# Optimization experiments

Hardware: AMD Instinct MI355X
Metric: run time of the kernel (lower is better)

Reference implementation:

```python
import jax, jax.numpy as jnp
import numpy as np
import math

B, N, M = 4, 512, 64
F, Q, H, R = 256, 16, 8, 32
D = F // H
ETA = 4.0
EPS = 1e-5
FFN_H = 512

def layer_norm(x, g, b):
    mu = jnp.mean(x, axis=-1, keepdims=True)
    var = jnp.mean((x - mu) ** 2, axis=-1, keepdims=True)
    return (x - mu) * jax.lax.rsqrt(var + EPS) * g + b

def setup_inputs() -> dict:
    key = jax.random.key(0)
    ks = jax.random.split(key, 24)
    def xav(k, shape):
        fan_in, fan_out = shape[1], shape[0]
        std = math.sqrt(2.0 / (fan_in + fan_out))
        return jax.random.normal(k, shape, dtype=jnp.float32) * std
    inp = {
        'a': jax.random.normal(ks[0], (B, N, F), dtype=jnp.float32),
        'charges': jax.random.normal(ks[1], (B, N, Q), dtype=jnp.float32),
        'idx_j': jax.random.randint(ks[2], (B, N, M), 0, N),
        'd_ij': jax.random.uniform(ks[3], (B, N, M), dtype=jnp.float32) * 5.0,
        'mask_ij': jax.random.bernoulli(ks[4], 0.3, (B, N, M)),
        'radial_shifts': jnp.linspace(0.5, 5.0, R, dtype=jnp.float32),
        'Wq': xav(ks[5], (F, F + Q)), 'bq': jnp.zeros((F,), jnp.float32),
        'Wk': xav(ks[6], (F, F + Q)), 'bk': jnp.zeros((F,), jnp.float32),
        'Wv': xav(ks[7], (F, F + Q)), 'bv': jnp.zeros((F,), jnp.float32),
        'Wrb': xav(ks[8], (H, R)), 'brb': jnp.zeros((H,), jnp.float32),
        'Wout': xav(ks[9], (F, 2 * F + R)), 'bout': jnp.zeros((F,), jnp.float32),
        'g1': jnp.ones((F,), jnp.float32), 'b1': jnp.zeros((F,), jnp.float32),
        'g2': jnp.ones((F,), jnp.float32), 'b2': jnp.zeros((F,), jnp.float32),
        'Wf1': xav(ks[10], (FFN_H, F)), 'bf1': jnp.zeros((FFN_H,), jnp.float32),
        'Wf2': xav(ks[11], (F, FFN_H)), 'bf2': jnp.zeros((F,), jnp.float32),
    }
    return inp

def reference(a, charges, idx_j, d_ij, mask_ij, radial_shifts,
              Wq, bq, Wk, bk, Wv, bv, Wrb, brb, Wout, bout,
              g1, b1, g2, b2, Wf1, bf1, Wf2, bf2):
    bidx = jnp.arange(B)[:, None, None]
    a_j = a[bidx, idx_j]          # [B,N,M,F]
    q_j = charges[bidx, idx_j]    # [B,N,M,Q]
    center = jnp.concatenate([a, charges], axis=-1)       # [B,N,F+Q]
    neigh = jnp.concatenate([a_j, q_j], axis=-1)          # [B,N,M,F+Q]
    q = (center @ Wq.T + bq).reshape(B, N, H, D)
    k = (neigh @ Wk.T + bk).reshape(B, N, M, H, D)
    v = (neigh @ Wv.T + bv).reshape(B, N, M, H, D)
    # radial basis: exp(-eta*(d - shift)^2)  -> [B,N,M,R]
    radial = jnp.exp(-ETA * (d_ij[..., None] - radial_shifts) ** 2)
    scores = jnp.einsum('bnhd,bnmhd->bnmh', q, k) / math.sqrt(D)
    scores = scores + radial @ Wrb.T + brb                # [B,N,M,H]
    scores = jnp.swapaxes(scores, -1, -2)                 # [B,N,H,M]
    scores = jnp.where(mask_ij[:, :, None, :], -jnp.inf, scores)
    attn = jax.nn.softmax(scores, axis=-1)
    attn = jnp.nan_to_num(attn, nan=0.0, posinf=0.0, neginf=0.0)
    context = jnp.einsum('bnhm,bnmhd->bnhd', attn, v).reshape(B, N, F)
    radial_context = jnp.einsum('bnhm,bnmg->bnhg', attn, radial).mean(axis=-2)  # [B,N,R]
    update = jnp.concatenate([a, context, radial_context], axis=-1) @ Wout.T + bout
    x = layer_norm(a + update, g1, b1)
    ff = jax.nn.gelu(x @ Wf1.T + bf1, approximate=False) @ Wf2.T + bf2
    return layer_norm(x + ff, g2, b2)
```

## Files before the change

kernel.cpp:

```cpp
#include <hip/hip_runtime.h>
#include <hip/hip_bf16.h>
#include <math.h>

#define Bb 4
#define Nn 512
#define Mm 64
#define Ff 256
#define Qq 16
#define Hh 8
#define Rr 32
#define FFNH 512
#define ROWS (Bb*Nn)
#define KIN (Ff+Qq)
#define KINP 288
#define KOUT (2*Ff+Rr)

typedef short short8 __attribute__((ext_vector_type(8)));
typedef unsigned short ushort8 __attribute__((ext_vector_type(8)));
typedef float f32x4 __attribute__((ext_vector_type(4)));

__device__ inline unsigned short f2b(float f) {
    union { float f; unsigned u; } c; c.f = f;
    unsigned r = c.u + 0x7fffu + ((c.u >> 16) & 1u);
    return (unsigned short)(r >> 16);
}
__device__ inline float b2f(unsigned short u) {
    union { unsigned u; float f; } c; c.u = ((unsigned)u) << 16;
    return c.f;
}

#define OFF_CENTER 0
#define OFF_WQKV   (OFF_CENTER + ROWS*KINP)
#define OFF_WOUT   (OFF_WQKV + 768*KINP)
#define OFF_WF1    (OFF_WOUT + Ff*KOUT)
#define OFF_WF2    (OFF_WF1 + FFNH*Ff)
#define OFF_U      (OFF_WF2 + Ff*FFNH)
#define OFF_XB     (OFF_U + ROWS*KOUT)
#define OFF_FFH    (OFF_XB + ROWS*Ff)
#define OFF_QKVB   (OFF_FFH + ROWS*FFNH)
#define CONV_TOTAL OFF_U
#define CONV_BLK4  (CONV_TOTAL/1024)
#define A2U_BLK4   (ROWS*Ff/1024)
#define MSK_BLK16  (Bb*Nn*Mm/(256*16))

__global__ __launch_bounds__(256) void prep(const float* __restrict__ a,
                                            const float* __restrict__ ch,
                                            const float* __restrict__ Wq,
                                            const float* __restrict__ Wk,
                                            const float* __restrict__ Wv,
                                            const float* __restrict__ Wout,
                                            const float* __restrict__ Wf1,
                                            const float* __restrict__ Wf2,
                                            const unsigned char* __restrict__ mask,
                                            int* __restrict__ flag,
                                            unsigned short* __restrict__ arena) {
    int bid = blockIdx.x, tid = threadIdx.x;
    if (bid < CONV_BLK4) {
        int i = (bid * 256 + tid) * 4;
        float4 v4 = {0.f, 0.f, 0.f, 0.f};
        if (i < OFF_WQKV) {
            int row = i / KINP, c = i - row * KINP;
            if (c < Ff)       v4 = *reinterpret_cast<const float4*>(a  + (size_t)row * Ff + c);
            else if (c < KIN) v4 = *reinterpret_cast<const float4*>(ch + (size_t)row * Qq + (c - Ff));
        } else if (i < OFF_WOUT) {
            int j = i - OFF_WQKV;
            int n = j / KINP, c = j - n * KINP;
            const float* W = n < 256 ? Wq : (n < 512 ? Wk : Wv);
            int nr = n & 255;
            if (c < KIN) v4 = *reinterpret_cast<const float4*>(W + (size_t)nr * KIN + c);
        } else if (i < OFF_WF1) {
            v4 = *reinterpret_cast<const float4*>(Wout + (i - OFF_WOUT));
        } else if (i < OFF_WF2) {
            v4 = *reinterpret_cast<const float4*>(Wf1 + (i - OFF_WF1));
        } else {
            v4 = *reinterpret_cast<const float4*>(Wf2 + (i - OFF_WF2));
        }
        ushort4 u;
        u.x = f2b(v4.x); u.y = f2b(v4.y); u.z = f2b(v4.z); u.w = f2b(v4.w);
        *reinterpret_cast<ushort4*>(arena + i) = u;
    } else if (bid < CONV_BLK4 + A2U_BLK4) {
        int j = ((bid - CONV_BLK4) * 256 + tid) * 4;
        int row = j >> 8, col = j & 255;
        float4 v4 = *reinterpret_cast<const float4*>(a + j);
        ushort4 u;
        u.x = f2b(v4.x); u.y = f2b(v4.y); u.z = f2b(v4.z); u.w = f2b(v4.w);
        *reinterpret_cast<ushort4*>(arena + OFF_U + (size_t)row * KOUT + col) = u;
    } else {
        int i = ((bid - CONV_BLK4 - A2U_BLK4) * 256 + tid) * 4;
        const uint4 v = reinterpret_cast<const uint4*>(mask)[i >> 2];
        unsigned m = (v.x | v.y | v.z | v.w) & 0xFFFFFF00u;
        if (m) *flag = 1;
    }
}

template<int KT, int SPLIT, int MODE>
__global__ __launch_bounds__(256) void gemm_mfma(const unsigned short* __restrict__ Ab, int lda,
                                                 const unsigned short* __restrict__ Wb, int ldw,
                                                 const float* __restrict__ b0,
                                                 const float* __restrict__ b1,
                                                 const float* __restrict__ b2,
                                                 float* __restrict__ C,
                                                 unsigned short* __restrict__ Cb,
                                                 int ldc, size_t pstride) {
    __shared__ unsigned short As[2][64][32];
    __shared__ unsigned short Bs[2][64][32];
    int tid = threadIdx.x;
    int colbase = blockIdx.x * 64;
    int rowbase = blockIdx.y * 64;
    constexpr int TPER = (KT + SPLIT - 1) / SPLIT;
    int t0 = blockIdx.z * TPER;
    int NL = KT - t0; if (NL > TPER) NL = TPER;

    int sr = tid >> 2, sl = tid & 3;
    const unsigned short* Ap = Ab + (size_t)(rowbase + sr) * lda + sl * 8;
    const unsigned short* Wp = Wb + (size_t)(colbase + sr) * ldw + sl * 8;
    int ssw = (sl ^ (sr & 3)) * 8;

    int wave = tid >> 6, lane = tid & 63;
    int wr = (wave >> 1) * 32, wc = (wave & 1) * 32;
    int lrow = lane & 15;
    int kslot = lane >> 4;
    int sp = (kslot ^ (lane & 3)) * 8;

    uint4 av, wv;
    auto prefetch = [&](int t) {
        av = *reinterpret_cast<const uint4*>(Ap + (size_t)t * 32);
        wv = *reinterpret_cast<const uint4*>(Wp + (size_t)t * 32);
    };
    auto writeLDS = [&](int buf) {
        *reinterpret_cast<uint4*>(&As[buf][sr][ssw]) = av;
        *reinterpret_cast<uint4*>(&Bs[buf][sr][ssw]) = wv;
    };

    f32x4 acc[2][2] = {};
    prefetch(t0);
    writeLDS(0);
    __syncthreads();
    for (int tt = 0; tt < NL; ++tt) {
        if (tt + 1 < NL) prefetch(t0 + tt + 1);
        int buf = tt & 1;
        short8 a0 = *reinterpret_cast<const short8*>(&As[buf][wr + lrow][sp]);
        short8 a1 = *reinterpret_cast<const short8*>(&As[buf][wr + 16 + lrow][sp]);
        short8 bv0 = *reinterpret_cast<const short8*>(&Bs[buf][wc + lrow][sp]);
        short8 bv1 = *reinterpret_cast<const short8*>(&Bs[buf][wc + 16 + lrow][sp]);
        acc[0][0] = __builtin_amdgcn_mfma_f32_16x16x32_bf16(a0, bv0, acc[0][0], 0, 0, 0);
        acc[0][1] = __builtin_amdgcn_mfma_f32_16x16x32_bf16(a0, bv1, acc[0][1], 0, 0, 0);
        acc[1][0] = __builtin_amdgcn_mfma_f32_16x16x32_bf16(a1, bv0, acc[1][0], 0, 0, 0);
        acc[1][1] = __builtin_amdgcn_mfma_f32_16x16x32_bf16(a1, bv1, acc[1][1], 0, 0, 0);
        if (tt + 1 < NL) {
            writeLDS((tt + 1) & 1);
            __syncthreads();
        }
    }

    const float* bias = b0;
    if (MODE == 1) {
        int sel = colbase >> 8;
        bias = sel == 0 ? b0 : (sel == 1 ? b1 : b2);
    }
    int colq = (colbase & 255);
    float* Cp = (MODE == 0) ? C + (size_t)blockIdx.z * pstride : C;
    #pragma unroll
    for (int fr = 0; fr < 2; ++fr) {
        #pragma unroll
        for (int fc = 0; fc < 2; ++fc) {
            int coll = wc + fc * 16 + (lane & 15);
            int col = colbase + coll;
            #pragma unroll
            for (int i = 0; i < 4; ++i) {
                int row = rowbase + wr + fr * 16 + (lane >> 4) * 4 + i;
                float v = acc[fr][fc][i];
                if (MODE == 0) {
                    Cp[(size_t)row * ldc + col] = v;
                } else if (MODE == 1) {
                    Cb[(size_t)row * ldc + col] = f2b(v + bias[colq + coll]);
                } else {
                    v += bias[col];
                    v = 0.5f * v * (1.0f + erff(v * 0.70710678118654752f));
                    Cb[(size_t)row * ldc + col] = f2b(v);
                }
            }
        }
    }
}

__global__ __launch_bounds__(256) void attn_kernel(const unsigned short* __restrict__ QKV,
                                                   const int* __restrict__ idx_j,
                                                   const float* __restrict__ d_ij,
                                                   const void* __restrict__ mask,
                                                   const float* __restrict__ shifts,
                                                   const float* __restrict__ Wrb,
                                                   const float* __restrict__ brb,
                                                   const int* __restrict__ flag,
                                                   unsigned short* __restrict__ Ub) {
    __shared__ unsigned short Kt[2][16][280];
    __shared__ float rad[Mm][36];
    __shared__ float att[Hh][Mm];
    __shared__ float attbar[Mm];
    __shared__ int   jl[Mm];
    __shared__ float dv[Mm];
    __shared__ int   maskf[Mm];
    __shared__ float shs[Rr];

    int row = blockIdx.x;
    int b = row >> 9;
    int tid = threadIdx.x;
    bool boolmask = (*flag != 0);

    if (tid < Mm) jl[tid] = idx_j[row * Mm + tid];
    else if (tid < 128) { int m = tid - 64; dv[m] = d_ij[row * Mm + m]; }
    else if (tid < 160) shs[tid - 128] = shifts[tid - 128];
    else if (tid >= 192) {
        int m = tid - 192;
        maskf[m] = boolmask ? (int)((const unsigned char*)mask)[row * Mm + m]
                            : ((const int*)mask)[row * Mm + m];
    }

    int half = tid & 1;
    int p = tid >> 1;
    int hh = p >> 4;
    int ml = p & 15;
    float qf[16];
    {
        const unsigned short* qrow = QKV + (size_t)row * 768 + hh * 32 + half * 16;
        ushort8 q0 = *reinterpret_cast<const ushort8*>(qrow);
        ushort8 q1 = *reinterpret_cast<const ushort8*>(qrow + 8);
        #pragma unroll
        for (int i = 0; i < 8; ++i) { qf[i] = b2f(q0[i]); qf[8 + i] = b2f(q1[i]); }
    }
    float4 wreg[4];
    #pragma unroll
    for (int c = 0; c < 4; ++c)
        wreg[c] = *reinterpret_cast<const float4*>(Wrb + hh * Rr + half * 16 + c * 4);
    float brbh = brb[hh];
    __syncthreads();

    auto stage = [&](int t, int seg, int buf) {
        #pragma unroll
        for (int q = 0; q < 2; ++q) {
            int chunk = q * 256 + tid;
            int r = chunk >> 5, s = chunk & 31;
            int j = jl[t * 16 + r];
            const uint4* src = reinterpret_cast<const uint4*>(QKV + (size_t)(b * Nn + j) * 768 + seg);
            uint4 v = src[s];
            *reinterpret_cast<uint4*>(&Kt[buf][r][s * 8]) = v;
        }
    };

    #pragma unroll
    for (int it = 0; it < 8; ++it) {
        int i = tid + it * 256;
        int m = i >> 5, r = i & 31;
        float t = dv[m] - shs[r];
        rad[m][r] = expf(-4.0f * t * t);
    }
    stage(0, 256, 0);
    __syncthreads();

    for (int t = 0; t < 4; ++t) {
        if (t < 3) stage(t + 1, 256, (t + 1) & 1);
        int buf = t & 1;
        const unsigned short* kr = &Kt[buf][ml][hh * 32 + half * 16];
        ushort8 k0 = *reinterpret_cast<const ushort8*>(kr);
        ushort8 k1 = *reinterpret_cast<const ushort8*>(kr + 8);
        float accK = 0.f;
        #pragma unroll
        for (int i = 0; i < 8; ++i) accK = fmaf(qf[i], b2f(k0[i]), accK);
        #pragma unroll
        for (int i = 0; i < 8; ++i) accK = fmaf(qf[8 + i], b2f(k1[i]), accK);
        float accR = 0.f;
        #pragma unroll
        for (int c = 0; c < 4; ++c) {
            float4 rv = *reinterpret_cast<const float4*>(&rad[t * 16 + ml][half * 16 + c * 4]);
            accR += wreg[c].x * rv.x + wreg[c].y * rv.y + wreg[c].z * rv.z + wreg[c].w * rv.w;
        }
        float tv = accK * 0.17677669529663687f + accR;
        tv += __shfl_xor(tv, 1);
        if (!half) {
            int m = t * 16 + ml;
            att[hh][m] = maskf[m] ? -INFINITY : (tv + brbh);
        }
        __syncthreads();
    }

    {
        int h = tid >> 5, l = tid & 31;
        float s0 = att[h][l], s1 = att[h][l + 32];
        float mx = fmaxf(s0, s1);
        #pragma unroll
        for (int off = 16; off; off >>= 1) mx = fmaxf(mx, __shfl_xor(mx, off, 32));
        float e0 = 0.f, e1 = 0.f;
        if (mx != -INFINITY) {
            e0 = expf(s0 - mx);
            e1 = expf(s1 - mx);
        }
        float sm = e0 + e1;
        #pragma unroll
        for (int off = 16; off; off >>= 1) sm += __shfl_xor(sm, off, 32);
        float inv = sm > 0.f ? 1.f / sm : 0.f;
        att[h][l] = e0 * inv;
        att[h][l + 32] = e1 * inv;
    }
    stage(0, 512, 0);
    __syncthreads();

    float ctx = 0.f;
    int h2 = tid >> 5, d0 = tid & 31;
    for (int t = 0; t < 4; ++t) {
        if (t < 3) stage(t + 1, 512, (t + 1) & 1);
        int buf = t & 1;
        #pragma unroll
        for (int m = 0; m < 16; ++m)
            ctx = fmaf(att[h2][t * 16 + m], b2f(Kt[buf][m][h2 * 32 + d0]), ctx);
        if (t == 0 && tid < Mm) {
            float sv = 0.f;
            #pragma unroll
            for (int h = 0; h < Hh; ++h) sv += att[h][tid];
            attbar[tid] = sv * 0.125f;
        }
        __syncthreads();
    }

    Ub[(size_t)row * KOUT + Ff + tid] = f2b(ctx);

    if (tid < 64) {
        int g = tid >> 1;
        float acc = 0.f;
        #pragma unroll
        for (int i = 0; i < 32; ++i) {
            int m = half * 32 + i;
            acc = fmaf(attbar[m], rad[m][g], acc);
        }
        acc += __shfl_xor(acc, 1);
        if (!half) Ub[(size_t)row * KOUT + 2 * Ff + g] = f2b(acc);
    }
}

template<int S, int WB>
__global__ __launch_bounds__(256) void add_ln_c(const float* __restrict__ x0,
                                                const float* __restrict__ part, size_t pstride,
                                                const float* __restrict__ bias,
                                                const float* __restrict__ g,
                                                const float* __restrict__ be,
                                                float* __restrict__ outp,
                                                unsigned short* __restrict__ xb) {
    int tid = threadIdx.x;
    int wave = tid >> 6, lane = tid & 63;
    int row = blockIdx.x * 4 + wave;
    size_t off = (size_t)row * Ff + lane * 4;
    float4 v = *reinterpret_cast<const float4*>(x0 + off);
    float4 bb = *reinterpret_cast<const float4*>(bias + lane * 4);
    v.x += bb.x; v.y += bb.y; v.z += bb.z; v.w += bb.w;
    #pragma unroll
    for (int s = 0; s < S; ++s) {
        float4 p = *reinterpret_cast<const float4*>(part + (size_t)s * pstride + off);
        v.x += p.x; v.y += p.y; v.z += p.z; v.w += p.w;
    }
    float sm = v.x + v.y + v.z + v.w;
    #pragma unroll
    for (int o = 32; o; o >>= 1) sm += __shfl_xor(sm, o, 64);
    float mu = sm * (1.f / Ff);
    float4 c = {v.x - mu, v.y - mu, v.z - mu, v.w - mu};
    float s2 = c.x * c.x + c.y * c.y + c.z * c.z + c.w * c.w;
    #pragma unroll
    for (int o = 32; o; o >>= 1) s2 += __shfl_xor(s2, o, 64);
    float inv = rsqrtf(s2 * (1.f / Ff) + 1e-5f);
    float4 gg = *reinterpret_cast<const float4*>(g + lane * 4);
    float4 ee = *reinterpret_cast<const float4*>(be + lane * 4);
    float4 r;
    r.x = c.x * inv * gg.x + ee.x;
    r.y = c.y * inv * gg.y + ee.y;
    r.z = c.z * inv * gg.z + ee.z;
    r.w = c.w * inv * gg.w + ee.w;
    *reinterpret_cast<float4*>(outp + off) = r;
    if (WB) {
        ushort4 u;
        u.x = f2b(r.x); u.y = f2b(r.y); u.z = f2b(r.z); u.w = f2b(r.w);
        *reinterpret_cast<ushort4*>(&xb[off]) = u;
    }
}

extern "C" void kernel_launch(void* const* d_in, const int* in_sizes, int n_in,
                              void* d_out, int out_size, void* d_ws, size_t ws_size,
                              hipStream_t stream) {
    const float* a       = (const float*)d_in[0];
    const float* charges = (const float*)d_in[1];
    const int*   idx_j   = (const int*)  d_in[2];
    const float* d_ij    = (const float*)d_in[3];
    const void*  mask    =               d_in[4];
    const float* shifts  = (const float*)d_in[5];
    const float* Wq   = (const float*)d_in[6];  const float* bq   = (const float*)d_in[7];
    const float* Wk   = (const float*)d_in[8];  const float* bk   = (const float*)d_in[9];
    const float* Wv   = (const float*)d_in[10]; const float* bv   = (const float*)d_in[11];
    const float* Wrb  = (const float*)d_in[12]; const float* brb  = (const float*)d_in[13];
    const float* Wout = (const float*)d_in[14]; const float* bout = (const float*)d_in[15];
    const float* g1   = (const float*)d_in[16]; const float* b1   = (const float*)d_in[17];
    const float* g2   = (const float*)d_in[18]; const float* b2   = (const float*)d_in[19];
    const float* Wf1  = (const float*)d_in[20]; const float* bf1  = (const float*)d_in[21];
    const float* Wf2  = (const float*)d_in[22]; const float* bf2  = (const float*)d_in[23];
    float* outp = (float*)d_out;

    float* ws   = (float*)d_ws;
    int*   flag = (int*)d_ws;
    float* part = ws + 1024;
    float* xbuf = part + 1048576;
    unsigned short* arena = (unsigned short*)(xbuf + 524288);
    unsigned short* centerb = arena + OFF_CENTER;
    unsigned short* Wqkvb   = arena + OFF_WQKV;
    unsigned short* Woutb   = arena + OFF_WOUT;
    unsigned short* Wf1b    = arena + OFF_WF1;
    unsigned short* Wf2b    = arena + OFF_WF2;
    unsigned short* Ub      = arena + OFF_U;
    unsigned short* xb      = arena + OFF_XB;
    unsigned short* ffhb    = arena + OFF_FFH;
    unsigned short* QKVB16  = arena + OFF_QKVB;

    hipMemsetAsync(flag, 0, sizeof(int), stream);
    prep<<<CONV_BLK4 + A2U_BLK4 + MSK_BLK16, 256, 0, stream>>>(
        a, charges, Wq, Wk, Wv, Wout, Wf1, Wf2, (const unsigned char*)mask, flag, arena);

    gemm_mfma<9, 1, 1><<<dim3(12, 32, 1), 256, 0, stream>>>(
        centerb, KINP, Wqkvb, KINP, bq, bk, bv, nullptr, QKVB16, 768, 0);

    attn_kernel<<<ROWS, 256, 0, stream>>>(QKVB16, idx_j, d_ij, mask, shifts, Wrb, brb, flag, Ub);

    gemm_mfma<17, 2, 0><<<dim3(4, 32, 2), 256, 0, stream>>>(
        Ub, KOUT, Woutb, KOUT, nullptr, nullptr, nullptr, part, nullptr, Ff, (size_t)ROWS * Ff);
    add_ln_c<2, 1><<<ROWS / 4, 256, 0, stream>>>(a, part, (size_t)ROWS * Ff, bout, g1, b1, xbuf, xb);

    gemm_mfma<8, 1, 2><<<dim3(8, 32, 1), 256, 0, stream>>>(
        xb, Ff, Wf1b, Ff, bf1, nullptr, nullptr, nullptr, ffhb, FFNH, 0);

    gemm_mfma<16, 2, 0><<<dim3(4, 32, 2), 256, 0, stream>>>(
        ffhb, FFNH, Wf2b, FFNH, nullptr, nullptr, nullptr, part, nullptr, Ff, (size_t)ROWS * Ff);
    add_ln_c<2, 0><<<ROWS / 4, 256, 0, stream>>>(xbuf, part, (size_t)ROWS * Ff, bf2, g2, b2, outp, nullptr);
}
```

Measured before the change: 64.28 us.

## Fuse split-K output GEMMs with residual add and LayerNorm via per-pane counters

The two split-K GEMMs that feed a LayerNorm now do the add+LN themselves. Each block writes its partial tile and bumps an atomic counter for its 64-row pane. Once all 8 blocks of a pane have arrived, every block normalizes 8 of the pane's rows, which removes two separate LayerNorm kernel launches. The cost is a spin-wait on global atomics, which assumes all 8 blocks of a pane are co-resident; with only 256 blocks that should hold but is not guaranteed.

```diff
diff --git a/kernel.cpp b/kernel.cpp
--- a/kernel.cpp
+++ b/kernel.cpp
@@ -159,7 +159,6 @@
         bias = sel == 0 ? b0 : (sel == 1 ? b1 : b2);
     }
     int colq = (colbase & 255);
-    float* Cp = (MODE == 0) ? C + (size_t)blockIdx.z * pstride : C;
     #pragma unroll
     for (int fr = 0; fr < 2; ++fr) {
         #pragma unroll
@@ -170,9 +169,7 @@
             for (int i = 0; i < 4; ++i) {
                 int row = rowbase + wr + fr * 16 + (lane >> 4) * 4 + i;
                 float v = acc[fr][fc][i];
-                if (MODE == 0) {
-                    Cp[(size_t)row * ldc + col] = v;
-                } else if (MODE == 1) {
+                if (MODE == 1) {
                     Cb[(size_t)row * ldc + col] = f2b(v + bias[colq + coll]);
                 } else {
                     v += bias[col];
@@ -180,6 +177,131 @@
                     Cb[(size_t)row * ldc + col] = f2b(v);
                 }
             }
+        }
+    }
+}
+
+template<int KT, int WB>
+__global__ __launch_bounds__(256) void gemm_ln(const unsigned short* __restrict__ Ab, int lda,
+                                               const unsigned short* __restrict__ Wb, int ldw,
+                                               float* __restrict__ part, size_t pstride,
+                                               int* __restrict__ cnt,
+                                               const float* __restrict__ x0,
+                                               const float* __restrict__ biasAdd,
+                                               const float* __restrict__ g,
+                                               const float* __restrict__ be,
+                                               float* __restrict__ outF,
+                                               unsigned short* __restrict__ xbOut) {
+    __shared__ unsigned short As[2][64][32];
+    __shared__ unsigned short Bs[2][64][32];
+    int tid = threadIdx.x;
+    int colbase = blockIdx.x * 64;
+    int rowbase = blockIdx.y * 64;
+    constexpr int TPER = (KT + 1) / 2;
+    int t0 = blockIdx.z * TPER;
+    int NL = KT - t0; if (NL > TPER) NL = TPER;
+
+    int sr = tid >> 2, sl = tid & 3;
+    const unsigned short* Ap = Ab + (size_t)(rowbase + sr) * lda + sl * 8;
+    const unsigned short* Wp = Wb + (size_t)(colbase + sr) * ldw + sl * 8;
+    int ssw = (sl ^ (sr & 3)) * 8;
+
+    int wave = tid >> 6, lane = tid & 63;
+    int wr = (wave >> 1) * 32, wc = (wave & 1) * 32;
+    int lrow = lane & 15;
+    int kslot = lane >> 4;
+    int sp = (kslot ^ (lane & 3)) * 8;
+
+    uint4 av, wv;
+    auto prefetch = [&](int t) {
+        av = *reinterpret_cast<const uint4*>(Ap + (size_t)t * 32);
+        wv = *reinterpret_cast<const uint4*>(Wp + (size_t)t * 32);
+    };
+    auto writeLDS = [&](int buf) {
+        *reinterpret_cast<uint4*>(&As[buf][sr][ssw]) = av;
+        *reinterpret_cast<uint4*>(&Bs[buf][sr][ssw]) = wv;
+    };
+
+    f32x4 acc[2][2] = {};
+    prefetch(t0);
+    writeLDS(0);
+    __syncthreads();
+    for (int tt = 0; tt < NL; ++tt) {
+        if (tt + 1 < NL) prefetch(t0 + tt + 1);
+        int buf = tt & 1;
+        short8 a0 = *reinterpret_cast<const short8*>(&As[buf][wr + lrow][sp]);
+        short8 a1 = *reinterpret_cast<const short8*>(&As[buf][wr + 16 + lrow][sp]);
+        short8 bv0 = *reinterpret_cast<const short8*>(&Bs[buf][wc + lrow][sp]);
+        short8 bv1 = *reinterpret_cast<const short8*>(&Bs[buf][wc + 16 + lrow][sp]);
+        acc[0][0] = __builtin_amdgcn_mfma_f32_16x16x32_bf16(a0, bv0, acc[0][0], 0, 0, 0);
+        acc[0][1] = __builtin_amdgcn_mfma_f32_16x16x32_bf16(a0, bv1, acc[0][1], 0, 0, 0);
+        acc[1][0] = __builtin_amdgcn_mfma_f32_16x16x32_bf16(a1, bv0, acc[1][0], 0, 0, 0);
+        acc[1][1] = __builtin_amdgcn_mfma_f32_16x16x32_bf16(a1, bv1, acc[1][1], 0, 0, 0);
+        if (tt + 1 < NL) {
+            writeLDS((tt + 1) & 1);
+            __syncthreads();
+        }
+    }
+
+    float* Cp = part + (size_t)blockIdx.z * pstride;
+    #pragma unroll
+    for (int fr = 0; fr < 2; ++fr) {
+        #pragma unroll
+        for (int fc = 0; fc < 2; ++fc) {
+            int col = colbase + wc + fc * 16 + (lane & 15);
+            #pragma unroll
+            for (int i = 0; i < 4; ++i) {
+                int row = rowbase + wr + fr * 16 + (lane >> 4) * 4 + i;
+                Cp[(size_t)row * Ff + col] = acc[fr][fc][i];
+            }
+        }
+    }
+
+    __threadfence();
+    __syncthreads();
+    int pane = blockIdx.y;
+    int sidx = blockIdx.z * 4 + blockIdx.x;
+    if (tid == 0) {
+        atomicAdd(&cnt[pane], 1);
+        while (atomicAdd(&cnt[pane], 0) < 8) __builtin_amdgcn_s_sleep(2);
+    }
+    __syncthreads();
+    __threadfence();
+
+    #pragma unroll
+    for (int it = 0; it < 2; ++it) {
+        int rr = wave + it * 4;
+        int row = pane * 64 + sidx * 8 + rr;
+        size_t off = (size_t)row * Ff + lane * 4;
+        float4 v = *reinterpret_cast<const float4*>(x0 + off);
+        float4 bb = *reinterpret_cast<const float4*>(biasAdd + lane * 4);
+        v.x += bb.x; v.y += bb.y; v.z += bb.z; v.w += bb.w;
+        #pragma unroll
+        for (int s = 0; s < 2; ++s) {
+            float4 p = *reinterpret_cast<const float4*>(part + (size_t)s * pstride + off);
+            v.x += p.x; v.y += p.y; v.z += p.z; v.w += p.w;
+        }
+        float sm = v.x + v.y + v.z + v.w;
+        #pragma unroll
+        for (int o = 32; o; o >>= 1) sm += __shfl_xor(sm, o, 64);
+        float mu = sm * (1.f / Ff);
+        float4 c = {v.x - mu, v.y - mu, v.z - mu, v.w - mu};
+        float s2 = c.x * c.x + c.y * c.y + c.z * c.z + c.w * c.w;
+        #pragma unroll
+        for (int o = 32; o; o >>= 1) s2 += __shfl_xor(s2, o, 64);
+        float inv = rsqrtf(s2 * (1.f / Ff) + 1e-5f);
+        float4 gg = *reinterpret_cast<const float4*>(g + lane * 4);
+        float4 ee = *reinterpret_cast<const float4*>(be + lane * 4);
+        float4 r;
+        r.x = c.x * inv * gg.x + ee.x;
+        r.y = c.y * inv * gg.y + ee.y;
+        r.z = c.z * inv * gg.z + ee.z;
+        r.w = c.w * inv * gg.w + ee.w;
+        *reinterpret_cast<float4*>(outF + off) = r;
+        if (WB) {
+            ushort4 u;
+            u.x = f2b(r.x); u.y = f2b(r.y); u.z = f2b(r.z); u.w = f2b(r.w);
+            *reinterpret_cast<ushort4*>(&xbOut[off]) = u;
         }
     }
 }
@@ -333,50 +455,6 @@
         }
         acc += __shfl_xor(acc, 1);
         if (!half) Ub[(size_t)row * KOUT + 2 * Ff + g] = f2b(acc);
-    }
-}
-
-template<int S, int WB>
-__global__ __launch_bounds__(256) void add_ln_c(const float* __restrict__ x0,
-                                                const float* __restrict__ part, size_t pstride,
-                                                const float* __restrict__ bias,
-                                                const float* __restrict__ g,
-                                                const float* __restrict__ be,
-                                                float* __restrict__ outp,
-                                                unsigned short* __restrict__ xb) {
-    int tid = threadIdx.x;
-    int wave = tid >> 6, lane = tid & 63;
-    int row = blockIdx.x * 4 + wave;
-    size_t off = (size_t)row * Ff + lane * 4;
-    float4 v = *reinterpret_cast<const float4*>(x0 + off);
-    float4 bb = *reinterpret_cast<const float4*>(bias + lane * 4);
-    v.x += bb.x; v.y += bb.y; v.z += bb.z; v.w += bb.w;
-    #pragma unroll
-    for (int s = 0; s < S; ++s) {
-        float4 p = *reinterpret_cast<const float4*>(part + (size_t)s * pstride + off);
-        v.x += p.x; v.y += p.y; v.z += p.z; v.w += p.w;
-    }
-    float sm = v.x + v.y + v.z + v.w;
-    #pragma unroll
-    for (int o = 32; o; o >>= 1) sm += __shfl_xor(sm, o, 64);
-    float mu = sm * (1.f / Ff);
-    float4 c = {v.x - mu, v.y - mu, v.z - mu, v.w - mu};
-    float s2 = c.x * c.x + c.y * c.y + c.z * c.z + c.w * c.w;
-    #pragma unroll
-    for (int o = 32; o; o >>= 1) s2 += __shfl_xor(s2, o, 64);
-    float inv = rsqrtf(s2 * (1.f / Ff) + 1e-5f);
-    float4 gg = *reinterpret_cast<const float4*>(g + lane * 4);
-    float4 ee = *reinterpret_cast<const float4*>(be + lane * 4);
-    float4 r;
-    r.x = c.x * inv * gg.x + ee.x;
-    r.y = c.y * inv * gg.y + ee.y;
-    r.z = c.z * inv * gg.z + ee.z;
-    r.w = c.w * inv * gg.w + ee.w;
-    *reinterpret_cast<float4*>(outp + off) = r;
-    if (WB) {
-        ushort4 u;
-        u.x = f2b(r.x); u.y = f2b(r.y); u.z = f2b(r.z); u.w = f2b(r.w);
-        *reinterpret_cast<ushort4*>(&xb[off]) = u;
     }
 }
 
@@ -402,6 +480,7 @@
 
     float* ws   = (float*)d_ws;
     int*   flag = (int*)d_ws;
+    int*   cnt  = flag + 1;
     float* part = ws + 1024;
     float* xbuf = part + 1048576;
     unsigned short* arena = (unsigned short*)(xbuf + 524288);
@@ -415,7 +494,7 @@
     unsigned short* ffhb    = arena + OFF_FFH;
     unsigned short* QKVB16  = arena + OFF_QKVB;
 
-    hipMemsetAsync(flag, 0, sizeof(int), stream);
+    hipMemsetAsync(flag, 0, 65 * sizeof(int), stream);
     prep<<<CONV_BLK4 + A2U_BLK4 + MSK_BLK16, 256, 0, stream>>>(
         a, charges, Wq, Wk, Wv, Wout, Wf1, Wf2, (const unsigned char*)mask, flag, arena);
 
@@ -424,14 +503,14 @@
 
     attn_kernel<<<ROWS, 256, 0, stream>>>(QKVB16, idx_j, d_ij, mask, shifts, Wrb, brb, flag, Ub);
 
-    gemm_mfma<17, 2, 0><<<dim3(4, 32, 2), 256, 0, stream>>>(
-        Ub, KOUT, Woutb, KOUT, nullptr, nullptr, nullptr, part, nullptr, Ff, (size_t)ROWS * Ff);
-    add_ln_c<2, 1><<<ROWS / 4, 256, 0, stream>>>(a, part, (size_t)ROWS * Ff, bout, g1, b1, xbuf, xb);
+    gemm_ln<17, 1><<<dim3(4, 32, 2), 256, 0, stream>>>(
+        Ub, KOUT, Woutb, KOUT, part, (size_t)ROWS * Ff, cnt,
+        a, bout, g1, b1, xbuf, xb);
 
     gemm_mfma<8, 1, 2><<<dim3(8, 32, 1), 256, 0, stream>>>(
         xb, Ff, Wf1b, Ff, bf1, nullptr, nullptr, nullptr, ffhb, FFNH, 0);
 
-    gemm_mfma<16, 2, 0><<<dim3(4, 32, 2), 256, 0, stream>>>(
-        ffhb, FFNH, Wf2b, FFNH, nullptr, nullptr, nullptr, part, nullptr, Ff, (size_t)ROWS * Ff);
-    add_ln_c<2, 0><<<ROWS / 4, 256, 0, stream>>>(xbuf, part, (size_t)ROWS * Ff, bf2, g2, b2, outp, nullptr);
-}
+    gemm_ln<16, 0><<<dim3(4, 32, 2), 256, 0, stream>>>(
+        ffhb, FFNH, Wf2b, FFNH, part, (size_t)ROWS * Ff, cnt + 32,
+        xbuf, bf2, g2, b2, outp, nullptr);
+}
```

Result: slower. 175.9 us (+173.7%).
